# Performance work log

Hardware: AMD Instinct MI355X
Metric: run time of the kernel (lower is better)

Reference implementation:

```python
import jax, jax.numpy as jnp
import numpy as np

B, S, H = 2, 2048, 1024
NUM_HEAD = 16
HEAD_HIDDEN = H // NUM_HEAD
SCALE = float(np.sqrt(HEAD_HIDDEN))  # 8.0
INF = 10000000000.0


def setup_inputs() -> dict:
    key = jax.random.key(0)
    ks = jax.random.split(key, 12)
    std = 1.0 / np.sqrt(H)
    mk = lambda k: (jax.random.normal(k, (H, H), jnp.float32) * std)
    return {
        "query": jax.random.normal(ks[0], (B, S, H), jnp.float32),
        "key": jax.random.normal(ks[1], (B, S, H), jnp.float32),
        "value": jax.random.normal(ks[2], (B, S, H), jnp.float32),
        "att_mask": jnp.ones((B, 1, 1, S), jnp.float32),
        "wq": mk(ks[3]), "bq": jnp.zeros((H,), jnp.float32),
        "wk": mk(ks[4]), "bk": jnp.zeros((H,), jnp.float32),
        "wv": mk(ks[5]), "bv": jnp.zeros((H,), jnp.float32),
        "wo": mk(ks[6]), "bo": jnp.zeros((H,), jnp.float32),
    }


def reference(query, key, value, att_mask, wq, bq, wk, bk, wv, bv, wo, bo):
    # projections (weights stored as [in, out])
    q = query @ wq + bq
    k = key @ wk + bk
    v = value @ wv + bv
    # split heads: [B, S, nH, hd]
    q = q.reshape(B, S, NUM_HEAD, HEAD_HIDDEN)
    k = k.reshape(B, S, NUM_HEAD, HEAD_HIDDEN)
    v = v.reshape(B, S, NUM_HEAD, HEAD_HIDDEN)
    # scores [B, nH, Sq, Sk], first divide by scale
    att = jnp.einsum("bqhd,bkhd->bhqk", q, k) / SCALE
    # additive mask applied BEFORE the second scale division (faithful quirk)
    att = att + (1.0 - att_mask) * (-INF)
    att = jax.nn.softmax(att / SCALE, axis=-1)
    out = jnp.einsum("bhqk,bkhd->bqhd", att, v).reshape(B, S, H)
    return out @ wo + bo
```

## Files before the change

### kernel.cpp

```cpp
#include <hip/hip_runtime.h>
#include <cstdint>

typedef unsigned short u16;
typedef __attribute__((ext_vector_type(8))) short bf16x8;
typedef __attribute__((ext_vector_type(4))) float f32x4;

#define S_LEN 2048
#define HDIM  1024
#define NHEAD 16

__device__ __forceinline__ float bf2f(u16 u){ return __uint_as_float(((uint32_t)u) << 16); }
__device__ __forceinline__ u16 f2bf(float f){
  uint32_t x = __float_as_uint(f);
  return (u16)((x + 0x7fffu + ((x >> 16) & 1u)) >> 16);
}

__device__ __forceinline__ void gload_lds16(const void* g, void* l){
  __builtin_amdgcn_global_load_lds((const __attribute__((address_space(1))) void*)g,
                                   (__attribute__((address_space(3))) void*)l, 16, 0, 0);
}

__global__ __launch_bounds__(256) void k_cvt3(const float* __restrict__ q, const float* __restrict__ k,
                                              const float* __restrict__ v, u16* __restrict__ oq,
                                              u16* __restrict__ ok, u16* __restrict__ ov){
  int z = blockIdx.y;
  const float* in = z == 0 ? q : (z == 1 ? k : v);
  u16* out = z == 0 ? oq : (z == 1 ? ok : ov);
  int i = blockIdx.x * 256 + threadIdx.x;
  float4 f0 = *(const float4*)&in[(size_t)i * 8];
  float4 f1 = *(const float4*)&in[(size_t)i * 8 + 4];
  bf16x8 o;
  o[0] = (short)f2bf(f0.x); o[1] = (short)f2bf(f0.y);
  o[2] = (short)f2bf(f0.z); o[3] = (short)f2bf(f0.w);
  o[4] = (short)f2bf(f1.x); o[5] = (short)f2bf(f1.y);
  o[6] = (short)f2bf(f1.z); o[7] = (short)f2bf(f1.w);
  *(bf16x8*)&out[(size_t)i * 8] = o;
}

__global__ __launch_bounds__(256) void k_tr_w4(const float* __restrict__ w0, const float* __restrict__ w1,
                                               const float* __restrict__ w2, const float* __restrict__ w3,
                                               u16* __restrict__ o0, u16* __restrict__ o1,
                                               u16* __restrict__ o2, u16* __restrict__ o3){
  int z = blockIdx.z;
  const float* in = z == 0 ? w0 : (z == 1 ? w1 : (z == 2 ? w2 : w3));
  u16* out = z == 0 ? o0 : (z == 1 ? o1 : (z == 2 ? o2 : o3));
  __shared__ float t[64][65];
  int r0 = threadIdx.x >> 6;
  int c  = threadIdx.x & 63;
  int bx = blockIdx.x * 64, by = blockIdx.y * 64;
  #pragma unroll
  for (int i = 0; i < 64; i += 4) t[r0 + i][c] = in[(size_t)(by + r0 + i) * 1024 + bx + c];
  __syncthreads();
  #pragma unroll
  for (int i = 0; i < 64; i += 4) out[(size_t)(bx + r0 + i) * 1024 + by + c] = f2bf(t[c][r0 + i]);
}

__global__ __launch_bounds__(256) void k_tr_v(const u16* __restrict__ v, u16* __restrict__ vt){
  __shared__ u16 t[64][65];
  int r0 = threadIdx.x >> 6, c = threadIdx.x & 63;
  int s0 = blockIdx.x * 64;
  int bh = blockIdx.y;
  int b = bh >> 4, h = bh & 15;
  const u16* src = v + (size_t)b * S_LEN * HDIM + h * 64;
  #pragma unroll
  for (int i = 0; i < 64; i += 4) t[r0 + i][c] = src[(size_t)(s0 + r0 + i) * HDIM + c];
  __syncthreads();
  u16* dst = vt + (size_t)bh * 64 * S_LEN + s0;
  #pragma unroll
  for (int i = 0; i < 64; i += 4) dst[(size_t)(r0 + i) * S_LEN + c] = t[c][r0 + i];
}

__global__ __launch_bounds__(256) void k_gemm_qkv(const u16* __restrict__ A0, const u16* __restrict__ A1,
                                                  const u16* __restrict__ A2,
                                                  const u16* __restrict__ W0, const u16* __restrict__ W1,
                                                  const u16* __restrict__ W2,
                                                  const float* __restrict__ b0, const float* __restrict__ b1,
                                                  const float* __restrict__ b2,
                                                  u16* __restrict__ C0, u16* __restrict__ C1,
                                                  u16* __restrict__ C2)
{
  int z = blockIdx.z;
  const u16* A  = z == 0 ? A0 : (z == 1 ? A1 : A2);
  const u16* Wt = z == 0 ? W0 : (z == 1 ? W1 : W2);
  const float* bias = z == 0 ? b0 : (z == 1 ? b1 : b2);
  u16* C = z == 0 ? C0 : (z == 1 ? C1 : C2);
  float scale = z == 0 ? (1.0f / 64.0f) : 1.0f;

  __shared__ u16 As[128 * 32];
  __shared__ u16 Bs[128 * 32];
  const int K = 1024, N = 1024;
  int tid = threadIdx.x;
  int lane = tid & 63, wave = tid >> 6;
  int quad = lane >> 4, c16 = lane & 15;
  int wm = wave >> 1, wn = wave & 1;
  int m0 = blockIdx.x * 128, n0 = blockIdx.y * 128;

  f32x4 acc[4][4] = {};

  for (int k0 = 0; k0 < K; k0 += 32) {
    #pragma unroll
    for (int i = 0; i < 2; i++) {
      int slot = tid + i * 256;
      int r = slot >> 2, cc = (slot & 3) * 8;
      gload_lds16(&A [(size_t)(m0 + r) * K + k0 + cc], &As[slot * 8]);
      gload_lds16(&Wt[(size_t)(n0 + r) * K + k0 + cc], &Bs[slot * 8]);
    }
    __syncthreads();
    bf16x8 af[4], bfr[4];
    #pragma unroll
    for (int mt = 0; mt < 4; mt++) af[mt]  = *(const bf16x8*)&As[(wm * 64 + mt * 16 + c16) * 32 + quad * 8];
    #pragma unroll
    for (int nt = 0; nt < 4; nt++) bfr[nt] = *(const bf16x8*)&Bs[(wn * 64 + nt * 16 + c16) * 32 + quad * 8];
    #pragma unroll
    for (int mt = 0; mt < 4; mt++)
      #pragma unroll
      for (int nt = 0; nt < 4; nt++)
        acc[mt][nt] = __builtin_amdgcn_mfma_f32_16x16x32_bf16(af[mt], bfr[nt], acc[mt][nt], 0, 0, 0);
    __syncthreads();
  }

  #pragma unroll
  for (int nt = 0; nt < 4; nt++) {
    int gc = n0 + wn * 64 + nt * 16 + c16;
    float bv = bias[gc];
    #pragma unroll
    for (int mt = 0; mt < 4; mt++)
      #pragma unroll
      for (int r = 0; r < 4; r++) {
        int gr = m0 + wm * 64 + mt * 16 + quad * 4 + r;
        C[(size_t)gr * N + gc] = f2bf((acc[mt][nt][r] + bv) * scale);
      }
  }
}

__global__ __launch_bounds__(256) void k_gemm_o(const u16* __restrict__ A, const u16* __restrict__ Wt,
                                                const float* __restrict__ bias, float* __restrict__ C)
{
  __shared__ u16 As[128 * 32];
  __shared__ u16 Bs[64 * 32];
  const int K = 1024, N = 1024;
  int tid = threadIdx.x;
  int lane = tid & 63, wave = tid >> 6;
  int quad = lane >> 4, c16 = lane & 15;
  int wm = wave >> 1, wn = wave & 1;
  int m0 = blockIdx.x * 128, n0 = blockIdx.y * 64;

  f32x4 acc[4][2] = {};

  for (int k0 = 0; k0 < K; k0 += 32) {
    #pragma unroll
    for (int i = 0; i < 2; i++) {
      int slot = tid + i * 256;
      int r = slot >> 2, cc = (slot & 3) * 8;
      gload_lds16(&A[(size_t)(m0 + r) * K + k0 + cc], &As[slot * 8]);
    }
    {
      int r = tid >> 2, cc = (tid & 3) * 8;
      gload_lds16(&Wt[(size_t)(n0 + r) * K + k0 + cc], &Bs[tid * 8]);
    }
    __syncthreads();
    bf16x8 af[4], bfr[2];
    #pragma unroll
    for (int mt = 0; mt < 4; mt++) af[mt]  = *(const bf16x8*)&As[(wm * 64 + mt * 16 + c16) * 32 + quad * 8];
    #pragma unroll
    for (int nt = 0; nt < 2; nt++) bfr[nt] = *(const bf16x8*)&Bs[(wn * 32 + nt * 16 + c16) * 32 + quad * 8];
    #pragma unroll
    for (int mt = 0; mt < 4; mt++)
      #pragma unroll
      for (int nt = 0; nt < 2; nt++)
        acc[mt][nt] = __builtin_amdgcn_mfma_f32_16x16x32_bf16(af[mt], bfr[nt], acc[mt][nt], 0, 0, 0);
    __syncthreads();
  }

  #pragma unroll
  for (int nt = 0; nt < 2; nt++) {
    int gc = n0 + wn * 32 + nt * 16 + c16;
    float bv = bias[gc];
    #pragma unroll
    for (int mt = 0; mt < 4; mt++)
      #pragma unroll
      for (int r = 0; r < 4; r++) {
        int gr = m0 + wm * 64 + mt * 16 + quad * 4 + r;
        C[(size_t)gr * N + gc] = acc[mt][nt][r] + bv;
      }
  }
}

__global__ __launch_bounds__(512, 4) void k_attn(const u16* __restrict__ Qm,
                                                 const u16* __restrict__ Km,
                                                 const u16* __restrict__ VTm,
                                                 const float* __restrict__ mask,
                                                 u16* __restrict__ Om)
{
  __shared__ u16 Ks[64][72];
  __shared__ u16 VTs[64][72];
  __shared__ u16 Ps[128][72];
  __shared__ float Ms[64];
  int tid = threadIdx.x;
  int lane = tid & 63, wave = tid >> 6;
  int quad = lane >> 4, c16 = lane & 15;
  int qb = blockIdx.x, h = blockIdx.y, b = blockIdx.z;
  const size_t SH = (size_t)S_LEN * HDIM;
  const u16* Qbase  = Qm + (size_t)b * SH + (size_t)qb * 128 * HDIM + h * 64;
  const u16* Kbase  = Km + (size_t)b * SH + h * 64;
  const u16* VTbase = VTm + (size_t)(b * NHEAD + h) * 64 * S_LEN;
  const float* Mbase = mask + (size_t)b * S_LEN;

  int qw0 = wave * 16;

  bf16x8 aq[2];
  #pragma unroll
  for (int kk = 0; kk < 2; kk++)
    aq[kk] = *(const bf16x8*)&Qbase[(size_t)(qw0 + c16) * HDIM + kk * 32 + quad * 8];

  f32x4 oacc[4] = {};
  float lsum[4] = {};

  for (int kt = 0; kt < S_LEN / 64; kt++) {
    int s0 = kt * 64;
    #pragma unroll
    for (int i = 0; i < 3; i++) {
      int c = i * 512 + tid;
      if (c < 576) {
        int r = c / 9, cc = c - r * 9;
        int col = (cc == 8) ? 0 : cc * 8;
        gload_lds16(&Kbase[(size_t)(s0 + r) * HDIM + col], &Ks[0][0] + c * 8);
      } else if (c < 1152) {
        int c2 = c - 576;
        int r = c2 / 9, cc = c2 - r * 9;
        int col = (cc == 8) ? 0 : cc * 8;
        gload_lds16(&VTbase[(size_t)r * S_LEN + s0 + col], &VTs[0][0] + c2 * 8);
      }
    }
    if (tid < 64) Ms[tid] = (1.0f - Mbase[s0 + tid]) * (-1.25e9f);
    __syncthreads();

    f32x4 sacc[4] = {};
    #pragma unroll
    for (int kk = 0; kk < 2; kk++) {
      bf16x8 bk[4];
      #pragma unroll
      for (int nt = 0; nt < 4; nt++) bk[nt] = *(const bf16x8*)&Ks[nt * 16 + c16][kk * 32 + quad * 8];
      #pragma unroll
      for (int nt = 0; nt < 4; nt++)
        sacc[nt] = __builtin_amdgcn_mfma_f32_16x16x32_bf16(aq[kk], bk[nt], sacc[nt], 0, 0, 0);
    }

    #pragma unroll
    for (int nt = 0; nt < 4; nt++) {
      float madd = Ms[nt * 16 + c16];
      #pragma unroll
      for (int r = 0; r < 4; r++) {
        float p = __expf(sacc[nt][r] + madd);
        lsum[r] += p;
        Ps[qw0 + quad * 4 + r][nt * 16 + c16] = f2bf(p);
      }
    }

    #pragma unroll
    for (int kk = 0; kk < 2; kk++) {
      bf16x8 pa = *(const bf16x8*)&Ps[qw0 + c16][kk * 32 + quad * 8];
      bf16x8 vb[4];
      #pragma unroll
      for (int nt = 0; nt < 4; nt++) vb[nt] = *(const bf16x8*)&VTs[nt * 16 + c16][kk * 32 + quad * 8];
      #pragma unroll
      for (int nt = 0; nt < 4; nt++)
        oacc[nt] = __builtin_amdgcn_mfma_f32_16x16x32_bf16(pa, vb[nt], oacc[nt], 0, 0, 0);
    }
    __syncthreads();
  }

  #pragma unroll
  for (int r = 0; r < 4; r++) {
    float v = lsum[r];
    v += __shfl_xor(v, 1); v += __shfl_xor(v, 2); v += __shfl_xor(v, 4); v += __shfl_xor(v, 8);
    lsum[r] = v;
  }

  u16* Obase = Om + (size_t)b * SH + (size_t)qb * 128 * HDIM + h * 64;
  #pragma unroll
  for (int nt = 0; nt < 4; nt++)
    #pragma unroll
    for (int r = 0; r < 4; r++) {
      int lr = qw0 + quad * 4 + r;
      Obase[(size_t)lr * HDIM + nt * 16 + c16] = f2bf(oacc[nt][r] / lsum[r]);
    }
}

extern "C" void kernel_launch(void* const* d_in, const int* in_sizes, int n_in,
                              void* d_out, int out_size, void* d_ws, size_t ws_size,
                              hipStream_t stream)
{
  (void)in_sizes; (void)n_in; (void)out_size; (void)ws_size;
  const float* q_in = (const float*)d_in[0];
  const float* k_in = (const float*)d_in[1];
  const float* v_in = (const float*)d_in[2];
  const float* mask = (const float*)d_in[3];
  const float* wq   = (const float*)d_in[4];
  const float* bq   = (const float*)d_in[5];
  const float* wk   = (const float*)d_in[6];
  const float* bk   = (const float*)d_in[7];
  const float* wv   = (const float*)d_in[8];
  const float* bv   = (const float*)d_in[9];
  const float* wo   = (const float*)d_in[10];
  const float* bo   = (const float*)d_in[11];

  u16* ws  = (u16*)d_ws;
  u16* wqt = ws;
  u16* wkt = wqt + (1u << 20);
  u16* wvt = wkt + (1u << 20);
  u16* wot = wvt + (1u << 20);
  u16* qi_ = wot + (1u << 20);
  u16* ki_ = qi_ + (4u << 20);
  u16* vi_ = ki_ + (4u << 20);
  u16* qb_ = vi_ + (4u << 20);
  u16* kb_ = qb_ + (4u << 20);
  u16* vb_ = kb_ + (4u << 20);
  u16* vtb = vb_ + (4u << 20);
  u16* ob_ = vtb + (4u << 20);

  dim3 blk(256);
  k_cvt3<<<dim3(2048, 3), blk, 0, stream>>>(q_in, k_in, v_in, qi_, ki_, vi_);
  k_tr_w4<<<dim3(16, 16, 4), blk, 0, stream>>>(wq, wk, wv, wo, wqt, wkt, wvt, wot);
  k_gemm_qkv<<<dim3(32, 8, 3), blk, 0, stream>>>(qi_, ki_, vi_, wqt, wkt, wvt, bq, bk, bv, qb_, kb_, vb_);
  k_tr_v<<<dim3(32, 32), blk, 0, stream>>>(vb_, vtb);
  k_attn<<<dim3(16, 16, 2), dim3(512), 0, stream>>>(qb_, kb_, vtb, mask, ob_);
  k_gemm_o<<<dim3(32, 16), blk, 0, stream>>>(ob_, wot, bo, (float*)d_out);
}
```

Before: 244.5 us.

## Fuse V transpose into QKV GEMM epilogue and give attention waves two query tiles

```diff
diff --git a/kernel.cpp b/kernel.cpp
--- a/kernel.cpp
+++ b/kernel.cpp
@@ -55,21 +55,6 @@
   for (int i = 0; i < 64; i += 4) out[(size_t)(bx + r0 + i) * 1024 + by + c] = f2bf(t[c][r0 + i]);
 }
 
-__global__ __launch_bounds__(256) void k_tr_v(const u16* __restrict__ v, u16* __restrict__ vt){
-  __shared__ u16 t[64][65];
-  int r0 = threadIdx.x >> 6, c = threadIdx.x & 63;
-  int s0 = blockIdx.x * 64;
-  int bh = blockIdx.y;
-  int b = bh >> 4, h = bh & 15;
-  const u16* src = v + (size_t)b * S_LEN * HDIM + h * 64;
-  #pragma unroll
-  for (int i = 0; i < 64; i += 4) t[r0 + i][c] = src[(size_t)(s0 + r0 + i) * HDIM + c];
-  __syncthreads();
-  u16* dst = vt + (size_t)bh * 64 * S_LEN + s0;
-  #pragma unroll
-  for (int i = 0; i < 64; i += 4) dst[(size_t)(r0 + i) * S_LEN + c] = t[c][r0 + i];
-}
-
 __global__ __launch_bounds__(256) void k_gemm_qkv(const u16* __restrict__ A0, const u16* __restrict__ A1,
                                                   const u16* __restrict__ A2,
                                                   const u16* __restrict__ W0, const u16* __restrict__ W1,
@@ -77,14 +62,12 @@
                                                   const float* __restrict__ b0, const float* __restrict__ b1,
                                                   const float* __restrict__ b2,
                                                   u16* __restrict__ C0, u16* __restrict__ C1,
-                                                  u16* __restrict__ C2)
+                                                  u16* __restrict__ vt)
 {
   int z = blockIdx.z;
   const u16* A  = z == 0 ? A0 : (z == 1 ? A1 : A2);
   const u16* Wt = z == 0 ? W0 : (z == 1 ? W1 : W2);
   const float* bias = z == 0 ? b0 : (z == 1 ? b1 : b2);
-  u16* C = z == 0 ? C0 : (z == 1 ? C1 : C2);
-  float scale = z == 0 ? (1.0f / 64.0f) : 1.0f;
 
   __shared__ u16 As[128 * 32];
   __shared__ u16 Bs[128 * 32];
@@ -119,17 +102,39 @@
     __syncthreads();
   }
 
-  #pragma unroll
-  for (int nt = 0; nt < 4; nt++) {
-    int gc = n0 + wn * 64 + nt * 16 + c16;
-    float bv = bias[gc];
-    #pragma unroll
-    for (int mt = 0; mt < 4; mt++)
-      #pragma unroll
-      for (int r = 0; r < 4; r++) {
-        int gr = m0 + wm * 64 + mt * 16 + quad * 4 + r;
-        C[(size_t)gr * N + gc] = f2bf((acc[mt][nt][r] + bv) * scale);
+  if (z == 2) {
+    #pragma unroll
+    for (int nt = 0; nt < 4; nt++) {
+      int gc = n0 + wn * 64 + nt * 16 + c16;
+      int h = gc >> 6, d = gc & 63;
+      float bv = bias[gc];
+      #pragma unroll
+      for (int mt = 0; mt < 4; mt++) {
+        int gr0 = m0 + wm * 64 + mt * 16 + quad * 4;
+        int bb = gr0 >> 11, s = gr0 & 2047;
+        ushort4 pk;
+        pk.x = f2bf(acc[mt][nt][0] + bv);
+        pk.y = f2bf(acc[mt][nt][1] + bv);
+        pk.z = f2bf(acc[mt][nt][2] + bv);
+        pk.w = f2bf(acc[mt][nt][3] + bv);
+        *(ushort4*)&vt[((size_t)(bb * NHEAD + h) * 64 + d) * S_LEN + s] = pk;
       }
+    }
+  } else {
+    float scale = z == 0 ? (1.0f / 64.0f) : 1.0f;
+    u16* C = z == 0 ? C0 : C1;
+    #pragma unroll
+    for (int nt = 0; nt < 4; nt++) {
+      int gc = n0 + wn * 64 + nt * 16 + c16;
+      float bv = bias[gc];
+      #pragma unroll
+      for (int mt = 0; mt < 4; mt++)
+        #pragma unroll
+        for (int r = 0; r < 4; r++) {
+          int gr = m0 + wm * 64 + mt * 16 + quad * 4 + r;
+          C[(size_t)gr * N + gc] = f2bf((acc[mt][nt][r] + bv) * scale);
+        }
+    }
   }
 }
 
@@ -186,7 +191,7 @@
   }
 }
 
-__global__ __launch_bounds__(512, 4) void k_attn(const u16* __restrict__ Qm,
+__global__ __launch_bounds__(256, 2) void k_attn(const u16* __restrict__ Qm,
                                                  const u16* __restrict__ Km,
                                                  const u16* __restrict__ VTm,
                                                  const float* __restrict__ mask,
@@ -206,21 +211,23 @@
   const u16* VTbase = VTm + (size_t)(b * NHEAD + h) * 64 * S_LEN;
   const float* Mbase = mask + (size_t)b * S_LEN;
 
-  int qw0 = wave * 16;
-
-  bf16x8 aq[2];
-  #pragma unroll
-  for (int kk = 0; kk < 2; kk++)
-    aq[kk] = *(const bf16x8*)&Qbase[(size_t)(qw0 + c16) * HDIM + kk * 32 + quad * 8];
-
-  f32x4 oacc[4] = {};
-  float lsum[4] = {};
+  int qw0 = wave * 32;
+
+  bf16x8 aq[2][2];
+  #pragma unroll
+  for (int mt = 0; mt < 2; mt++)
+    #pragma unroll
+    for (int kk = 0; kk < 2; kk++)
+      aq[mt][kk] = *(const bf16x8*)&Qbase[(size_t)(qw0 + mt * 16 + c16) * HDIM + kk * 32 + quad * 8];
+
+  f32x4 oacc[2][4] = {};
+  float lsum[2][4] = {};
 
   for (int kt = 0; kt < S_LEN / 64; kt++) {
     int s0 = kt * 64;
     #pragma unroll
-    for (int i = 0; i < 3; i++) {
-      int c = i * 512 + tid;
+    for (int i = 0; i < 5; i++) {
+      int c = i * 256 + tid;
       if (c < 576) {
         int r = c / 9, cc = c - r * 9;
         int col = (cc == 8) ? 0 : cc * 8;
@@ -235,56 +242,67 @@
     if (tid < 64) Ms[tid] = (1.0f - Mbase[s0 + tid]) * (-1.25e9f);
     __syncthreads();
 
-    f32x4 sacc[4] = {};
+    f32x4 sacc[2][4] = {};
     #pragma unroll
     for (int kk = 0; kk < 2; kk++) {
       bf16x8 bk[4];
       #pragma unroll
       for (int nt = 0; nt < 4; nt++) bk[nt] = *(const bf16x8*)&Ks[nt * 16 + c16][kk * 32 + quad * 8];
       #pragma unroll
-      for (int nt = 0; nt < 4; nt++)
-        sacc[nt] = __builtin_amdgcn_mfma_f32_16x16x32_bf16(aq[kk], bk[nt], sacc[nt], 0, 0, 0);
+      for (int mt = 0; mt < 2; mt++)
+        #pragma unroll
+        for (int nt = 0; nt < 4; nt++)
+          sacc[mt][nt] = __builtin_amdgcn_mfma_f32_16x16x32_bf16(aq[mt][kk], bk[nt], sacc[mt][nt], 0, 0, 0);
     }
 
     #pragma unroll
     for (int nt = 0; nt < 4; nt++) {
       float madd = Ms[nt * 16 + c16];
       #pragma unroll
+      for (int mt = 0; mt < 2; mt++)
+        #pragma unroll
+        for (int r = 0; r < 4; r++) {
+          float p = __expf(sacc[mt][nt][r] + madd);
+          lsum[mt][r] += p;
+          Ps[qw0 + mt * 16 + quad * 4 + r][nt * 16 + c16] = f2bf(p);
+        }
+    }
+
+    #pragma unroll
+    for (int kk = 0; kk < 2; kk++) {
+      bf16x8 pa[2], vb[4];
+      #pragma unroll
+      for (int mt = 0; mt < 2; mt++) pa[mt] = *(const bf16x8*)&Ps[qw0 + mt * 16 + c16][kk * 32 + quad * 8];
+      #pragma unroll
+      for (int nt = 0; nt < 4; nt++) vb[nt] = *(const bf16x8*)&VTs[nt * 16 + c16][kk * 32 + quad * 8];
+      #pragma unroll
+      for (int mt = 0; mt < 2; mt++)
+        #pragma unroll
+        for (int nt = 0; nt < 4; nt++)
+          oacc[mt][nt] = __builtin_amdgcn_mfma_f32_16x16x32_bf16(pa[mt], vb[nt], oacc[mt][nt], 0, 0, 0);
+    }
+    __syncthreads();
+  }
+
+  #pragma unroll
+  for (int mt = 0; mt < 2; mt++)
+    #pragma unroll
+    for (int r = 0; r < 4; r++) {
+      float v = lsum[mt][r];
+      v += __shfl_xor(v, 1); v += __shfl_xor(v, 2); v += __shfl_xor(v, 4); v += __shfl_xor(v, 8);
+      lsum[mt][r] = v;
+    }
+
+  u16* Obase = Om + (size_t)b * SH + (size_t)qb * 128 * HDIM + h * 64;
+  #pragma unroll
+  for (int mt = 0; mt < 2; mt++)
+    #pragma unroll
+    for (int nt = 0; nt < 4; nt++)
+      #pragma unroll
       for (int r = 0; r < 4; r++) {
-        float p = __expf(sacc[nt][r] + madd);
-        lsum[r] += p;
-        Ps[qw0 + quad * 4 + r][nt * 16 + c16] = f2bf(p);
+        int lr = qw0 + mt * 16 + quad * 4 + r;
+        Obase[(size_t)lr * HDIM + nt * 16 + c16] = f2bf(oacc[mt][nt][r] / lsum[mt][r]);
       }
-    }
-
-    #pragma unroll
-    for (int kk = 0; kk < 2; kk++) {
-      bf16x8 pa = *(const bf16x8*)&Ps[qw0 + c16][kk * 32 + quad * 8];
-      bf16x8 vb[4];
-      #pragma unroll
-      for (int nt = 0; nt < 4; nt++) vb[nt] = *(const bf16x8*)&VTs[nt * 16 + c16][kk * 32 + quad * 8];
-      #pragma unroll
-      for (int nt = 0; nt < 4; nt++)
-        oacc[nt] = __builtin_amdgcn_mfma_f32_16x16x32_bf16(pa, vb[nt], oacc[nt], 0, 0, 0);
-    }
-    __syncthreads();
-  }
-
-  #pragma unroll
-  for (int r = 0; r < 4; r++) {
-    float v = lsum[r];
-    v += __shfl_xor(v, 1); v += __shfl_xor(v, 2); v += __shfl_xor(v, 4); v += __shfl_xor(v, 8);
-    lsum[r] = v;
-  }
-
-  u16* Obase = Om + (size_t)b * SH + (size_t)qb * 128 * HDIM + h * 64;
-  #pragma unroll
-  for (int nt = 0; nt < 4; nt++)
-    #pragma unroll
-    for (int r = 0; r < 4; r++) {
-      int lr = qw0 + quad * 4 + r;
-      Obase[(size_t)lr * HDIM + nt * 16 + c16] = f2bf(oacc[nt][r] / lsum[r]);
-    }
 }
 
 extern "C" void kernel_launch(void* const* d_in, const int* in_sizes, int n_in,
@@ -315,15 +333,13 @@
   u16* vi_ = ki_ + (4u << 20);
   u16* qb_ = vi_ + (4u << 20);
   u16* kb_ = qb_ + (4u << 20);
-  u16* vb_ = kb_ + (4u << 20);
-  u16* vtb = vb_ + (4u << 20);
+  u16* vtb = kb_ + (4u << 20);
   u16* ob_ = vtb + (4u << 20);
 
   dim3 blk(256);
   k_cvt3<<<dim3(2048, 3), blk, 0, stream>>>(q_in, k_in, v_in, qi_, ki_, vi_);
   k_tr_w4<<<dim3(16, 16, 4), blk, 0, stream>>>(wq, wk, wv, wo, wqt, wkt, wvt, wot);
-  k_gemm_qkv<<<dim3(32, 8, 3), blk, 0, stream>>>(qi_, ki_, vi_, wqt, wkt, wvt, bq, bk, bv, qb_, kb_, vb_);
-  k_tr_v<<<dim3(32, 32), blk, 0, stream>>>(vb_, vtb);
-  k_attn<<<dim3(16, 16, 2), dim3(512), 0, stream>>>(qb_, kb_, vtb, mask, ob_);
+  k_gemm_qkv<<<dim3(32, 8, 3), blk, 0, stream>>>(qi_, ki_, vi_, wqt, wkt, wvt, bq, bk, bv, qb_, kb_, vtb);
+  k_attn<<<dim3(16, 16, 2), blk, 0, stream>>>(qb_, kb_, vtb, mask, ob_);
   k_gemm_o<<<dim3(32, 16), blk, 0, stream>>>(ob_, wot, bo, (float*)d_out);
 }
```

Result: slower. 252.3 us (+3.2%).
